# Kernel tuning notes

Measured on AMD Instinct MI355X. Metric: run time of the kernel, lower is better.

Reference implementation:

```python
import jax, jax.numpy as jnp
import numpy as np

N_NODES = 50000
N_EDGES = 800000
IN_DIM = 128
OUT_DIM = 128
NUM_HEADS = 8
HEAD_DIM = OUT_DIM // NUM_HEADS
LN_EPS = 1e-5


def setup_inputs() -> dict:
    key = jax.random.key(0)
    ks = jax.random.split(key, 8)
    # xavier-uniform bounds
    def xavier(k, shape, fan_in, fan_out):
        a = float(np.sqrt(6.0 / (fan_in + fan_out)))
        return jax.random.uniform(k, shape, jnp.float32, -a, a)
    x = jax.random.normal(ks[0], (N_NODES, IN_DIM), jnp.float32)
    edge_index = jax.random.randint(ks[1], (2, N_EDGES), 0, N_NODES, jnp.int32)
    # store Linear weights as (in, out) so forward is x @ W (same math as torch x @ W.T)
    W_src = xavier(ks[2], (IN_DIM, OUT_DIM), IN_DIM, OUT_DIM)
    W_dst = xavier(ks[3], (IN_DIM, OUT_DIM), IN_DIM, OUT_DIM)
    attn = xavier(ks[4], (NUM_HEADS, HEAD_DIM), HEAD_DIM, NUM_HEADS)
    W_out = xavier(ks[5], (OUT_DIM, OUT_DIM), OUT_DIM, OUT_DIM)
    b_out = jnp.zeros((OUT_DIM,), jnp.float32)
    gamma = jnp.ones((OUT_DIM,), jnp.float32)
    beta = jnp.zeros((OUT_DIM,), jnp.float32)
    return {"x": x, "edge_index": edge_index, "W_src": W_src, "W_dst": W_dst,
            "attn": attn, "W_out": W_out, "b_out": b_out, "gamma": gamma, "beta": beta}


def reference(x, edge_index, W_src, W_dst, attn, W_out, b_out, gamma, beta):
    N = x.shape[0]
    H, D = attn.shape
    src, dst = edge_index[0], edge_index[1]
    # node transforms: (N, H, D)
    h_src = (x @ W_src).reshape(N, H, D)
    h_dst = (x @ W_dst).reshape(N, H, D)
    # per-edge GATv2 attention logits (E, H)
    h_src_e = h_src[src]                                  # (E, H, D)
    e = jax.nn.leaky_relu(h_src_e + h_dst[dst], 0.2)
    s = jnp.einsum('ehd,hd->eh', e, attn)
    # segment (scatter) softmax over incoming edges of each dst node
    m = jax.ops.segment_max(s, dst, num_segments=N)       # (N, H)
    exp = jnp.exp(s - m[dst])
    denom = jax.ops.segment_sum(exp, dst, num_segments=N)
    alpha = exp / (denom[dst] + 1e-8)                     # (E, H)
    # weighted message aggregation
    msg = (h_src_e * alpha[..., None]).reshape(-1, H * D)
    out = jax.ops.segment_sum(msg, dst, num_segments=N)   # (N, H*D)
    out = out @ W_out + b_out
    out = out + x                                          # residual (in_dim == out_dim)
    # LayerNorm
    mu = jnp.mean(out, axis=-1, keepdims=True)
    var = jnp.var(out, axis=-1, keepdims=True)
    out = (out - mu) * jax.lax.rsqrt(var + LN_EPS) * gamma + beta
    return out
```

## Files before the change

kernel.cpp:

```cpp
#include <hip/hip_runtime.h>
#include <hip/hip_bf16.h>

#define HEADS 8
#define CDIM 128
#define CAP 96
#define CHUNK 2048
#define CSTR 16
#define LOG2E 1.44269504088896f

typedef __attribute__((ext_vector_type(8))) short bf16x8;
typedef __attribute__((ext_vector_type(4))) float f32x4;
typedef __attribute__((ext_vector_type(2))) _Float16 h16x2;

__device__ __forceinline__ unsigned short f2bs(float f) {
    union { __hip_bfloat16 b; unsigned short u; } c;
    c.b = __float2bfloat16(f);
    return c.u;
}

__device__ __forceinline__ unsigned short f2hs(float f) {
    union { _Float16 h; unsigned short u; } c;
    c.h = (_Float16)f;
    return c.u;
}

__global__ __launch_bounds__(256) void init_kernel(
        int* __restrict__ cnt,
        const float* __restrict__ Wsrc,
        const float* __restrict__ Wdst,
        const float* __restrict__ Wout,
        unsigned short* __restrict__ WT,
        unsigned short* __restrict__ WoT, int N, int nzblk) {
    const int b = blockIdx.x;
    if (b < nzblk) {
        const int i = b * 256 + threadIdx.x;
        if (i < N * CSTR) cnt[i] = 0;
        return;
    }
    const int i = (b - nzblk) * 256 + threadIdx.x;
    if (i < 16384)      { WT[i] = f2bs(Wsrc[(i & 127) * CDIM + (i >> 7)]); }
    else if (i < 32768) { int j = i - 16384; WT[16384 + j] = f2bs(Wdst[(j & 127) * CDIM + (j >> 7)]); }
    else if (i < 49152) { int j = i - 32768; WoT[j] = f2bs(Wout[(j & 127) * CDIM + (j >> 7)]); }
}

__global__ __launch_bounds__(256) void fused_bucket_transform3(
        const int* __restrict__ ei,
        int* __restrict__ cnt,
        int* __restrict__ bucket,
        const float* __restrict__ x,
        const unsigned short* __restrict__ WT,
        unsigned short* __restrict__ hsrc,
        unsigned short* __restrict__ hdst,
        int N, int E, int ngemm, int nbucket) {
    const int g = blockIdx.x;
    const bool is_gemm = ((g % 5) == 4) && ((g / 5) < ngemm);
    if (!is_gemm) {
        const int bid = g - g / 5;
        if (bid >= nbucket) return;
        const int shard = bid & 7;
        const int base = (bid >> 3) * CHUNK + (int)threadIdx.x;
        int d[8], s[8];
#pragma unroll
        for (int q = 0; q < 8; q++) {
            const int idx = base + q * 256;
            const int safe = idx < E ? idx : 0;
            d[q] = ei[E + safe];
            s[q] = ei[safe];
        }
        bool act[8];
        int pos[8];
#pragma unroll
        for (int q = 0; q < 8; q++) {
            const int idx = base + q * 256;
            act[q] = (idx < E) && ((d[q] & 7) == shard);
            pos[q] = CAP;
            if (act[q]) pos[q] = atomicAdd(&cnt[(size_t)d[q] * CSTR], 1);
        }
#pragma unroll
        for (int q = 0; q < 8; q++) {
            if (act[q] && pos[q] < CAP) bucket[(size_t)d[q] * CAP + pos[q]] = s[q];
        }
        return;
    }
    __shared__ unsigned short As[64][136];
    __shared__ unsigned short Bs[128][136];
    const int t = threadIdx.x;
    const int m0 = (g / 5) * 64;
    for (int i = t; i < 64 * 32; i += 256) {
        const int r = i >> 5, kq = i & 31;
        const int gr = m0 + r;
        float4 v = make_float4(0.f, 0.f, 0.f, 0.f);
        if (gr < N) v = *(const float4*)(x + (size_t)gr * CDIM + kq * 4);
        uint2 pk;
        pk.x = (unsigned)f2bs(v.x) | ((unsigned)f2bs(v.y) << 16);
        pk.y = (unsigned)f2bs(v.z) | ((unsigned)f2bs(v.w) << 16);
        *(uint2*)&As[r][kq * 4] = pk;
    }
    const int w = t >> 6, lane = t & 63, l16 = lane & 15, quad = lane >> 4;
    const int wm = (w & 1) * 32, wn = (w >> 1) * 64;
#pragma unroll
    for (int half = 0; half < 2; half++) {
        const unsigned short* Wb = WT + (size_t)half * 16384;
        for (int i = t; i < 128 * 16; i += 256) {
            const int r = i >> 4, q = i & 15;
            *(uint4*)&Bs[r][q * 8] = *(const uint4*)(Wb + (size_t)r * CDIM + q * 8);
        }
        __syncthreads();
        f32x4 acc[2][4];
#pragma unroll
        for (int mi = 0; mi < 2; mi++)
#pragma unroll
            for (int ni = 0; ni < 4; ni++) acc[mi][ni] = (f32x4){0.f, 0.f, 0.f, 0.f};
#pragma unroll
        for (int kc = 0; kc < 4; kc++) {
            const int k0 = kc * 32 + quad * 8;
            bf16x8 af[2], bf[4];
            af[0] = *(const bf16x8*)&As[wm + l16][k0];
            af[1] = *(const bf16x8*)&As[wm + 16 + l16][k0];
#pragma unroll
            for (int ni = 0; ni < 4; ni++)
                bf[ni] = *(const bf16x8*)&Bs[wn + ni * 16 + l16][k0];
#pragma unroll
            for (int mi = 0; mi < 2; mi++)
#pragma unroll
                for (int ni = 0; ni < 4; ni++)
                    acc[mi][ni] = __builtin_amdgcn_mfma_f32_16x16x32_bf16(af[mi], bf[ni], acc[mi][ni], 0, 0, 0);
        }
        unsigned short* H = half ? hdst : hsrc;
#pragma unroll
        for (int mi = 0; mi < 2; mi++)
#pragma unroll
            for (int reg = 0; reg < 4; reg++) {
                const int gm = m0 + wm + mi * 16 + quad * 4 + reg;
                if (gm < N) {
#pragma unroll
                    for (int ni = 0; ni < 4; ni++)
                        H[(size_t)gm * CDIM + wn + ni * 16 + l16] = f2hs(acc[mi][ni][reg]);
                }
            }
        __syncthreads();
    }
}

__global__ __launch_bounds__(256) void attn_agg6(
        const unsigned short* __restrict__ hsrc,
        const unsigned short* __restrict__ hdst,
        const float* __restrict__ attn,
        const int* __restrict__ cnt,
        const int* __restrict__ bucket,
        unsigned short* __restrict__ aggb) {
    __shared__ int src_lds[4][CAP];
    const int t = threadIdx.x;
    const int w = t >> 6, lane = t & 63;
    const int dst = blockIdx.x * 4 + w;
    int deg = cnt[(size_t)dst * CSTR];
    deg = deg > CAP ? CAP : deg;
    for (int j = lane; j < deg; j += 64)
        src_lds[w][j] = bucket[(size_t)dst * CAP + j];

    const int l32 = lane & 31;
    const int eh = lane >> 5;
    const uint2 hdu = *(const uint2*)(hdst + (size_t)dst * CDIM + l32 * 4);
    const h16x2 hd01 = __builtin_bit_cast(h16x2, hdu.x);
    const h16x2 hd23 = __builtin_bit_cast(h16x2, hdu.y);
    const float4 a4 = ((const float4*)attn)[l32];
    h16x2 a01, a23;
    a01[0] = (_Float16)(a4.x * LOG2E); a01[1] = (_Float16)(a4.y * LOG2E);
    a23[0] = (_Float16)(a4.z * LOG2E); a23[1] = (_Float16)(a4.w * LOG2E);
    const h16x2 k02 = { (_Float16)0.2f, (_Float16)0.2f };

    const unsigned short* hb = hsrc + l32 * 4;

    float l = 0.f, acc0 = 0.f, acc1 = 0.f, acc2 = 0.f, acc3 = 0.f;
    for (int j0 = 0; j0 < deg; j0 += 8) {
        uint2 vv[4];
#pragma unroll
        for (int p = 0; p < 4; p++) {
            const int j = j0 + 2 * p + eh;
            const int sj = (j < deg) ? src_lds[w][j] : 0;
            vv[p] = *(const uint2*)(hb + (size_t)sj * CDIM);
        }
#pragma unroll
        for (int p = 0; p < 4; p++) {
            const int j = j0 + 2 * p + eh;
            const h16x2 v01 = __builtin_bit_cast(h16x2, vv[p].x);
            const h16x2 v23 = __builtin_bit_cast(h16x2, vv[p].y);
            h16x2 e01 = v01 + hd01;
            h16x2 e23 = v23 + hd23;
            e01 = __builtin_elementwise_max(e01, e01 * k02);
            e23 = __builtin_elementwise_max(e23, e23 * k02);
            float pp = __builtin_amdgcn_fdot2(e01, a01, 0.f, false);
            pp = __builtin_amdgcn_fdot2(e23, a23, pp, false);
            pp += __int_as_float(__builtin_amdgcn_update_dpp(0, __float_as_int(pp), 0xB1, 0xF, 0xF, true));
            pp += __int_as_float(__builtin_amdgcn_update_dpp(0, __float_as_int(pp), 0x4E, 0xF, 0xF, true));
            float wgt = __builtin_amdgcn_exp2f(pp);
            wgt = (j < deg) ? wgt : 0.f;
            l += wgt;
            acc0 = fmaf(wgt, (float)v01[0], acc0);
            acc1 = fmaf(wgt, (float)v01[1], acc1);
            acc2 = fmaf(wgt, (float)v23[0], acc2);
            acc3 = fmaf(wgt, (float)v23[1], acc3);
        }
    }
    l    += __shfl_xor(l, 32);
    acc0 += __shfl_xor(acc0, 32);
    acc1 += __shfl_xor(acc1, 32);
    acc2 += __shfl_xor(acc2, 32);
    acc3 += __shfl_xor(acc3, 32);
    if (lane < 32) {
        const float r = 1.f / (l + 1e-8f);
        uint2 o;
        o.x = (unsigned)f2bs(acc0 * r) | ((unsigned)f2bs(acc1 * r) << 16);
        o.y = (unsigned)f2bs(acc2 * r) | ((unsigned)f2bs(acc3 * r) << 16);
        *(uint2*)(aggb + (size_t)dst * CDIM + l32 * 4) = o;
    }
}

__global__ __launch_bounds__(256) void out_mfma_ln64(
        const unsigned short* __restrict__ aggb,
        const float* __restrict__ x,
        const unsigned short* __restrict__ WoT,
        const float* __restrict__ bo,
        const float* __restrict__ gam,
        const float* __restrict__ bet,
        float* __restrict__ out, int N) {
    __shared__ unsigned short As[64][136];
    __shared__ unsigned short Bs[128][136];
    __shared__ float red1[64][2], red2[64][2];
    __shared__ float s_mu[64], s_rs[64];
    const int t = threadIdx.x;
    const int m0 = blockIdx.x * 64;
    for (int i = t; i < 64 * 16; i += 256) {
        const int r = i >> 4, q = i & 15;
        const int gr = m0 + r;
        uint4 v = make_uint4(0u, 0u, 0u, 0u);
        if (gr < N) v = *(const uint4*)(aggb + (size_t)gr * CDIM + q * 8);
        *(uint4*)&As[r][q * 8] = v;
    }
    for (int i = t; i < 128 * 16; i += 256) {
        const int r = i >> 4, q = i & 15;
        *(uint4*)&Bs[r][q * 8] = *(const uint4*)(WoT + (size_t)r * CDIM + q * 8);
    }
    __syncthreads();
    const int w = t >> 6, lane = t & 63, l16 = lane & 15, quad = lane >> 4;
    const int wm = (w & 1) * 32, wn = (w >> 1) * 64;
    f32x4 acc[2][4];
#pragma unroll
    for (int mi = 0; mi < 2; mi++)
#pragma unroll
        for (int ni = 0; ni < 4; ni++) acc[mi][ni] = (f32x4){0.f, 0.f, 0.f, 0.f};
#pragma unroll
    for (int kc = 0; kc < 4; kc++) {
        const int k0 = kc * 32 + quad * 8;
        bf16x8 af[2], bf[4];
        af[0] = *(const bf16x8*)&As[l16 + wm][k0];
        af[1] = *(const bf16x8*)&As[l16 + wm + 16][k0];
#pragma unroll
        for (int ni = 0; ni < 4; ni++)
            bf[ni] = *(const bf16x8*)&Bs[wn + ni * 16 + l16][k0];
#pragma unroll
        for (int mi = 0; mi < 2; mi++)
#pragma unroll
            for (int ni = 0; ni < 4; ni++)
                acc[mi][ni] = __builtin_amdgcn_mfma_f32_16x16x32_bf16(af[mi], bf[ni], acc[mi][ni], 0, 0, 0);
    }
    float bi[4], g4[4], be4[4];
#pragma unroll
    for (int ni = 0; ni < 4; ni++) {
        const int n = wn + ni * 16 + l16;
        bi[ni] = bo[n]; g4[ni] = gam[n]; be4[ni] = bet[n];
    }
#pragma unroll
    for (int mi = 0; mi < 2; mi++)
#pragma unroll
        for (int reg = 0; reg < 4; reg++) {
            const int gm = m0 + wm + mi * 16 + quad * 4 + reg;
#pragma unroll
            for (int ni = 0; ni < 4; ni++) {
                const float xr = (gm < N) ? x[(size_t)gm * CDIM + wn + ni * 16 + l16] : 0.f;
                acc[mi][ni][reg] += bi[ni] + xr;
            }
        }
#pragma unroll
    for (int mi = 0; mi < 2; mi++)
#pragma unroll
        for (int reg = 0; reg < 4; reg++) {
            float s1 = acc[mi][0][reg] + acc[mi][1][reg] + acc[mi][2][reg] + acc[mi][3][reg];
            float s2 = acc[mi][0][reg] * acc[mi][0][reg] + acc[mi][1][reg] * acc[mi][1][reg]
                     + acc[mi][2][reg] * acc[mi][2][reg] + acc[mi][3][reg] * acc[mi][3][reg];
            s1 += __shfl_xor(s1, 1, 16); s1 += __shfl_xor(s1, 2, 16);
            s1 += __shfl_xor(s1, 4, 16); s1 += __shfl_xor(s1, 8, 16);
            s2 += __shfl_xor(s2, 1, 16); s2 += __shfl_xor(s2, 2, 16);
            s2 += __shfl_xor(s2, 4, 16); s2 += __shfl_xor(s2, 8, 16);
            if (l16 == 0) {
                const int row = wm + mi * 16 + quad * 4 + reg;
                red1[row][w >> 1] = s1;
                red2[row][w >> 1] = s2;
            }
        }
    __syncthreads();
    if (t < 64) {
        const float s1 = red1[t][0] + red1[t][1];
        const float s2 = red2[t][0] + red2[t][1];
        const float mu = s1 * (1.f / 128.f);
        const float var = s2 * (1.f / 128.f) - mu * mu;
        s_mu[t] = mu;
        s_rs[t] = rsqrtf(var + 1e-5f);
    }
    __syncthreads();
#pragma unroll
    for (int mi = 0; mi < 2; mi++)
#pragma unroll
        for (int reg = 0; reg < 4; reg++) {
            const int row = wm + mi * 16 + quad * 4 + reg;
            const int gm = m0 + row;
            if (gm < N) {
                const float mu = s_mu[row], rs = s_rs[row];
#pragma unroll
                for (int ni = 0; ni < 4; ni++)
                    out[(size_t)gm * CDIM + wn + ni * 16 + l16] =
                        (acc[mi][ni][reg] - mu) * rs * g4[ni] + be4[ni];
            }
        }
}

extern "C" void kernel_launch(void* const* d_in, const int* in_sizes, int n_in,
                              void* d_out, int out_size, void* d_ws, size_t ws_size,
                              hipStream_t stream) {
    const float* x    = (const float*)d_in[0];
    const int*   ei   = (const int*)d_in[1];
    const float* Wsrc = (const float*)d_in[2];
    const float* Wdst = (const float*)d_in[3];
    const float* attn = (const float*)d_in[4];
    const float* Wout = (const float*)d_in[5];
    const float* bo   = (const float*)d_in[6];
    const float* gam  = (const float*)d_in[7];
    const float* bet  = (const float*)d_in[8];
    float* out = (float*)d_out;

    const int N = in_sizes[0] / CDIM;
    const int E = in_sizes[1] / 2;
    const int NX = N * CDIM;

    unsigned short* hsrc_h = (unsigned short*)d_ws;
    unsigned short* hdst_h = hsrc_h + (size_t)NX;
    unsigned short* aggb   = hdst_h + (size_t)NX;
    unsigned short* WT     = aggb + (size_t)NX;
    unsigned short* WoT    = WT + 32768;
    int* cnt    = (int*)(WoT + 16384);
    int* bucket = cnt + (size_t)N * CSTR;

    const int nzblk    = (N * CSTR + 255) / 256;
    const int nwblk    = 49152 / 256;
    const int ngroups  = (E + CHUNK - 1) / CHUNK;
    const int nbucket  = ngroups * 8;
    const int ngemm    = (N + 63) / 64;

    init_kernel<<<nzblk + nwblk, 256, 0, stream>>>(cnt, Wsrc, Wdst, Wout, WT, WoT, N, nzblk);
    fused_bucket_transform3<<<nbucket + ngemm, 256, 0, stream>>>(
        ei, cnt, bucket, x, WT, hsrc_h, hdst_h, N, E, ngemm, nbucket);
    attn_agg6<<<N / 4, 256, 0, stream>>>(hsrc_h, hdst_h, attn, cnt, bucket, aggb);
    out_mfma_ln64<<<(N + 63) / 64, 256, 0, stream>>>(aggb, x, WoT, bo, gam, bet, out, N);
}
```

Baseline: 187.1 us.

## Fuse attention aggregation with output GEMM and LayerNorm kernel

Merges the per-destination attention aggregation kernel into the output projection + LayerNorm kernel, keeping aggregated rows in LDS instead of writing them to global memory. Each wave now loops over 16 destination nodes sequentially, and the output GEMM is restructured so each wave owns 16 rows across all 128 columns, eliminating cross-wave LayerNorm reductions. This removes a kernel launch and the intermediate bf16 round trip, but greatly reduces the number of blocks and serializes the latency-bound gathers within each wave.

```diff
diff --git a/kernel.cpp b/kernel.cpp
--- a/kernel.cpp
+++ b/kernel.cpp
@@ -142,82 +142,12 @@
     }
 }
 
-__global__ __launch_bounds__(256) void attn_agg6(
+__global__ __launch_bounds__(256, 4) void attn_out_fused(
         const unsigned short* __restrict__ hsrc,
         const unsigned short* __restrict__ hdst,
         const float* __restrict__ attn,
         const int* __restrict__ cnt,
         const int* __restrict__ bucket,
-        unsigned short* __restrict__ aggb) {
-    __shared__ int src_lds[4][CAP];
-    const int t = threadIdx.x;
-    const int w = t >> 6, lane = t & 63;
-    const int dst = blockIdx.x * 4 + w;
-    int deg = cnt[(size_t)dst * CSTR];
-    deg = deg > CAP ? CAP : deg;
-    for (int j = lane; j < deg; j += 64)
-        src_lds[w][j] = bucket[(size_t)dst * CAP + j];
-
-    const int l32 = lane & 31;
-    const int eh = lane >> 5;
-    const uint2 hdu = *(const uint2*)(hdst + (size_t)dst * CDIM + l32 * 4);
-    const h16x2 hd01 = __builtin_bit_cast(h16x2, hdu.x);
-    const h16x2 hd23 = __builtin_bit_cast(h16x2, hdu.y);
-    const float4 a4 = ((const float4*)attn)[l32];
-    h16x2 a01, a23;
-    a01[0] = (_Float16)(a4.x * LOG2E); a01[1] = (_Float16)(a4.y * LOG2E);
-    a23[0] = (_Float16)(a4.z * LOG2E); a23[1] = (_Float16)(a4.w * LOG2E);
-    const h16x2 k02 = { (_Float16)0.2f, (_Float16)0.2f };
-
-    const unsigned short* hb = hsrc + l32 * 4;
-
-    float l = 0.f, acc0 = 0.f, acc1 = 0.f, acc2 = 0.f, acc3 = 0.f;
-    for (int j0 = 0; j0 < deg; j0 += 8) {
-        uint2 vv[4];
-#pragma unroll
-        for (int p = 0; p < 4; p++) {
-            const int j = j0 + 2 * p + eh;
-            const int sj = (j < deg) ? src_lds[w][j] : 0;
-            vv[p] = *(const uint2*)(hb + (size_t)sj * CDIM);
-        }
-#pragma unroll
-        for (int p = 0; p < 4; p++) {
-            const int j = j0 + 2 * p + eh;
-            const h16x2 v01 = __builtin_bit_cast(h16x2, vv[p].x);
-            const h16x2 v23 = __builtin_bit_cast(h16x2, vv[p].y);
-            h16x2 e01 = v01 + hd01;
-            h16x2 e23 = v23 + hd23;
-            e01 = __builtin_elementwise_max(e01, e01 * k02);
-            e23 = __builtin_elementwise_max(e23, e23 * k02);
-            float pp = __builtin_amdgcn_fdot2(e01, a01, 0.f, false);
-            pp = __builtin_amdgcn_fdot2(e23, a23, pp, false);
-            pp += __int_as_float(__builtin_amdgcn_update_dpp(0, __float_as_int(pp), 0xB1, 0xF, 0xF, true));
-            pp += __int_as_float(__builtin_amdgcn_update_dpp(0, __float_as_int(pp), 0x4E, 0xF, 0xF, true));
-            float wgt = __builtin_amdgcn_exp2f(pp);
-            wgt = (j < deg) ? wgt : 0.f;
-            l += wgt;
-            acc0 = fmaf(wgt, (float)v01[0], acc0);
-            acc1 = fmaf(wgt, (float)v01[1], acc1);
-            acc2 = fmaf(wgt, (float)v23[0], acc2);
-            acc3 = fmaf(wgt, (float)v23[1], acc3);
-        }
-    }
-    l    += __shfl_xor(l, 32);
-    acc0 += __shfl_xor(acc0, 32);
-    acc1 += __shfl_xor(acc1, 32);
-    acc2 += __shfl_xor(acc2, 32);
-    acc3 += __shfl_xor(acc3, 32);
-    if (lane < 32) {
-        const float r = 1.f / (l + 1e-8f);
-        uint2 o;
-        o.x = (unsigned)f2bs(acc0 * r) | ((unsigned)f2bs(acc1 * r) << 16);
-        o.y = (unsigned)f2bs(acc2 * r) | ((unsigned)f2bs(acc3 * r) << 16);
-        *(uint2*)(aggb + (size_t)dst * CDIM + l32 * 4) = o;
-    }
-}
-
-__global__ __launch_bounds__(256) void out_mfma_ln64(
-        const unsigned short* __restrict__ aggb,
         const float* __restrict__ x,
         const unsigned short* __restrict__ WoT,
         const float* __restrict__ bo,
@@ -225,102 +155,139 @@
         const float* __restrict__ bet,
         float* __restrict__ out, int N) {
     __shared__ unsigned short As[64][136];
-    __shared__ unsigned short Bs[128][136];
-    __shared__ float red1[64][2], red2[64][2];
-    __shared__ float s_mu[64], s_rs[64];
+    __shared__ unsigned short Bs[64][136];
+    __shared__ int src_lds[4][CAP];
     const int t = threadIdx.x;
+    const int w = t >> 6, lane = t & 63, l16 = lane & 15, quad = lane >> 4;
+    const int l32 = lane & 31, eh = lane >> 5;
     const int m0 = blockIdx.x * 64;
-    for (int i = t; i < 64 * 16; i += 256) {
-        const int r = i >> 4, q = i & 15;
-        const int gr = m0 + r;
-        uint4 v = make_uint4(0u, 0u, 0u, 0u);
-        if (gr < N) v = *(const uint4*)(aggb + (size_t)gr * CDIM + q * 8);
-        *(uint4*)&As[r][q * 8] = v;
-    }
-    for (int i = t; i < 128 * 16; i += 256) {
-        const int r = i >> 4, q = i & 15;
-        *(uint4*)&Bs[r][q * 8] = *(const uint4*)(WoT + (size_t)r * CDIM + q * 8);
-    }
-    __syncthreads();
-    const int w = t >> 6, lane = t & 63, l16 = lane & 15, quad = lane >> 4;
-    const int wm = (w & 1) * 32, wn = (w >> 1) * 64;
-    f32x4 acc[2][4];
-#pragma unroll
-    for (int mi = 0; mi < 2; mi++)
-#pragma unroll
-        for (int ni = 0; ni < 4; ni++) acc[mi][ni] = (f32x4){0.f, 0.f, 0.f, 0.f};
-#pragma unroll
-    for (int kc = 0; kc < 4; kc++) {
-        const int k0 = kc * 32 + quad * 8;
-        bf16x8 af[2], bf[4];
-        af[0] = *(const bf16x8*)&As[l16 + wm][k0];
-        af[1] = *(const bf16x8*)&As[l16 + wm + 16][k0];
-#pragma unroll
-        for (int ni = 0; ni < 4; ni++)
-            bf[ni] = *(const bf16x8*)&Bs[wn + ni * 16 + l16][k0];
-#pragma unroll
-        for (int mi = 0; mi < 2; mi++)
+    const int gm0 = m0 + w * 16;
+
+    const float4 a4 = ((const float4*)attn)[l32];
+    h16x2 a01, a23;
+    a01[0] = (_Float16)(a4.x * LOG2E); a01[1] = (_Float16)(a4.y * LOG2E);
+    a23[0] = (_Float16)(a4.z * LOG2E); a23[1] = (_Float16)(a4.w * LOG2E);
+    const h16x2 k02 = { (_Float16)0.2f, (_Float16)0.2f };
+    const unsigned short* hb = hsrc + l32 * 4;
+
+    for (int i = 0; i < 16; i++) {
+        const int dst = gm0 + i;
+        if (dst >= N) break;
+        int deg = cnt[(size_t)dst * CSTR];
+        deg = deg > CAP ? CAP : deg;
+        for (int j = lane; j < deg; j += 64)
+            src_lds[w][j] = bucket[(size_t)dst * CAP + j];
+
+        const uint2 hdu = *(const uint2*)(hdst + (size_t)dst * CDIM + l32 * 4);
+        const h16x2 hd01 = __builtin_bit_cast(h16x2, hdu.x);
+        const h16x2 hd23 = __builtin_bit_cast(h16x2, hdu.y);
+
+        float l = 0.f, acc0 = 0.f, acc1 = 0.f, acc2 = 0.f, acc3 = 0.f;
+        for (int j0 = 0; j0 < deg; j0 += 8) {
+            uint2 vv[4];
+#pragma unroll
+            for (int p = 0; p < 4; p++) {
+                const int j = j0 + 2 * p + eh;
+                const int sj = (j < deg) ? src_lds[w][j] : 0;
+                vv[p] = *(const uint2*)(hb + (size_t)sj * CDIM);
+            }
+#pragma unroll
+            for (int p = 0; p < 4; p++) {
+                const int j = j0 + 2 * p + eh;
+                const h16x2 v01 = __builtin_bit_cast(h16x2, vv[p].x);
+                const h16x2 v23 = __builtin_bit_cast(h16x2, vv[p].y);
+                h16x2 e01 = v01 + hd01;
+                h16x2 e23 = v23 + hd23;
+                e01 = __builtin_elementwise_max(e01, e01 * k02);
+                e23 = __builtin_elementwise_max(e23, e23 * k02);
+                float pp = __builtin_amdgcn_fdot2(e01, a01, 0.f, false);
+                pp = __builtin_amdgcn_fdot2(e23, a23, pp, false);
+                pp += __int_as_float(__builtin_amdgcn_update_dpp(0, __float_as_int(pp), 0xB1, 0xF, 0xF, true));
+                pp += __int_as_float(__builtin_amdgcn_update_dpp(0, __float_as_int(pp), 0x4E, 0xF, 0xF, true));
+                float wgt = __builtin_amdgcn_exp2f(pp);
+                wgt = (j < deg) ? wgt : 0.f;
+                l += wgt;
+                acc0 = fmaf(wgt, (float)v01[0], acc0);
+                acc1 = fmaf(wgt, (float)v01[1], acc1);
+                acc2 = fmaf(wgt, (float)v23[0], acc2);
+                acc3 = fmaf(wgt, (float)v23[1], acc3);
+            }
+        }
+        l    += __shfl_xor(l, 32);
+        acc0 += __shfl_xor(acc0, 32);
+        acc1 += __shfl_xor(acc1, 32);
+        acc2 += __shfl_xor(acc2, 32);
+        acc3 += __shfl_xor(acc3, 32);
+        if (lane < 32) {
+            const float r = 1.f / (l + 1e-8f);
+            uint2 o;
+            o.x = (unsigned)f2bs(acc0 * r) | ((unsigned)f2bs(acc1 * r) << 16);
+            o.y = (unsigned)f2bs(acc2 * r) | ((unsigned)f2bs(acc3 * r) << 16);
+            *(uint2*)&As[w * 16 + i][l32 * 4] = o;
+        }
+    }
+
+    bf16x8 af[4];
+#pragma unroll
+    for (int kc = 0; kc < 4; kc++)
+        af[kc] = *(const bf16x8*)&As[w * 16 + l16][kc * 32 + quad * 8];
+    f32x4 acc[8];
+#pragma unroll
+    for (int a = 0; a < 8; a++) acc[a] = (f32x4){0.f, 0.f, 0.f, 0.f};
+#pragma unroll
+    for (int nb = 0; nb < 2; nb++) {
+        if (nb) __syncthreads();
+        for (int i = t; i < 64 * 16; i += 256) {
+            const int r = i >> 4, q = i & 15;
+            *(uint4*)&Bs[r][q * 8] = *(const uint4*)(WoT + (size_t)(nb * 64 + r) * CDIM + q * 8);
+        }
+        __syncthreads();
+#pragma unroll
+        for (int kc = 0; kc < 4; kc++) {
+            const int k0 = kc * 32 + quad * 8;
+            bf16x8 bf[4];
 #pragma unroll
             for (int ni = 0; ni < 4; ni++)
-                acc[mi][ni] = __builtin_amdgcn_mfma_f32_16x16x32_bf16(af[mi], bf[ni], acc[mi][ni], 0, 0, 0);
-    }
-    float bi[4], g4[4], be4[4];
-#pragma unroll
-    for (int ni = 0; ni < 4; ni++) {
-        const int n = wn + ni * 16 + l16;
-        bi[ni] = bo[n]; g4[ni] = gam[n]; be4[ni] = bet[n];
-    }
-#pragma unroll
-    for (int mi = 0; mi < 2; mi++)
+                bf[ni] = *(const bf16x8*)&Bs[ni * 16 + l16][k0];
+#pragma unroll
+            for (int ni = 0; ni < 4; ni++)
+                acc[nb * 4 + ni] = __builtin_amdgcn_mfma_f32_16x16x32_bf16(af[kc], bf[ni], acc[nb * 4 + ni], 0, 0, 0);
+        }
+    }
+    float g4[8], be4[8];
+#pragma unroll
+    for (int a = 0; a < 8; a++) {
+        const int n = a * 16 + l16;
+        const float bi = bo[n]; g4[a] = gam[n]; be4[a] = bet[n];
 #pragma unroll
         for (int reg = 0; reg < 4; reg++) {
-            const int gm = m0 + wm + mi * 16 + quad * 4 + reg;
-#pragma unroll
-            for (int ni = 0; ni < 4; ni++) {
-                const float xr = (gm < N) ? x[(size_t)gm * CDIM + wn + ni * 16 + l16] : 0.f;
-                acc[mi][ni][reg] += bi[ni] + xr;
-            }
-        }
-#pragma unroll
-    for (int mi = 0; mi < 2; mi++)
+            const int gm = gm0 + quad * 4 + reg;
+            const float xr = (gm < N) ? x[(size_t)gm * CDIM + n] : 0.f;
+            acc[a][reg] += bi + xr;
+        }
+    }
+    float mu4[4], rs4[4];
+#pragma unroll
+    for (int reg = 0; reg < 4; reg++) {
+        float s1 = 0.f, s2 = 0.f;
+#pragma unroll
+        for (int a = 0; a < 8; a++) { s1 += acc[a][reg]; s2 += acc[a][reg] * acc[a][reg]; }
+        s1 += __shfl_xor(s1, 1, 16); s1 += __shfl_xor(s1, 2, 16);
+        s1 += __shfl_xor(s1, 4, 16); s1 += __shfl_xor(s1, 8, 16);
+        s2 += __shfl_xor(s2, 1, 16); s2 += __shfl_xor(s2, 2, 16);
+        s2 += __shfl_xor(s2, 4, 16); s2 += __shfl_xor(s2, 8, 16);
+        const float mu = s1 * (1.f / 128.f);
+        mu4[reg] = mu;
+        rs4[reg] = rsqrtf(s2 * (1.f / 128.f) - mu * mu + 1e-5f);
+    }
+#pragma unroll
+    for (int a = 0; a < 8; a++)
 #pragma unroll
         for (int reg = 0; reg < 4; reg++) {
-            float s1 = acc[mi][0][reg] + acc[mi][1][reg] + acc[mi][2][reg] + acc[mi][3][reg];
-            float s2 = acc[mi][0][reg] * acc[mi][0][reg] + acc[mi][1][reg] * acc[mi][1][reg]
-                     + acc[mi][2][reg] * acc[mi][2][reg] + acc[mi][3][reg] * acc[mi][3][reg];
-            s1 += __shfl_xor(s1, 1, 16); s1 += __shfl_xor(s1, 2, 16);
-            s1 += __shfl_xor(s1, 4, 16); s1 += __shfl_xor(s1, 8, 16);
-            s2 += __shfl_xor(s2, 1, 16); s2 += __shfl_xor(s2, 2, 16);
-            s2 += __shfl_xor(s2, 4, 16); s2 += __shfl_xor(s2, 8, 16);
-            if (l16 == 0) {
-                const int row = wm + mi * 16 + quad * 4 + reg;
-                red1[row][w >> 1] = s1;
-                red2[row][w >> 1] = s2;
-            }
-        }
-    __syncthreads();
-    if (t < 64) {
-        const float s1 = red1[t][0] + red1[t][1];
-        const float s2 = red2[t][0] + red2[t][1];
-        const float mu = s1 * (1.f / 128.f);
-        const float var = s2 * (1.f / 128.f) - mu * mu;
-        s_mu[t] = mu;
-        s_rs[t] = rsqrtf(var + 1e-5f);
-    }
-    __syncthreads();
-#pragma unroll
-    for (int mi = 0; mi < 2; mi++)
-#pragma unroll
-        for (int reg = 0; reg < 4; reg++) {
-            const int row = wm + mi * 16 + quad * 4 + reg;
-            const int gm = m0 + row;
-            if (gm < N) {
-                const float mu = s_mu[row], rs = s_rs[row];
-#pragma unroll
-                for (int ni = 0; ni < 4; ni++)
-                    out[(size_t)gm * CDIM + wn + ni * 16 + l16] =
-                        (acc[mi][ni][reg] - mu) * rs * g4[ni] + be4[ni];
-            }
+            const int gm = gm0 + quad * 4 + reg;
+            if (gm < N)
+                out[(size_t)gm * CDIM + a * 16 + l16] =
+                    (acc[a][reg] - mu4[reg]) * rs4[reg] * g4[a] + be4[a];
         }
 }
 
@@ -349,6 +316,7 @@
     unsigned short* WoT    = WT + 32768;
     int* cnt    = (int*)(WoT + 16384);
     int* bucket = cnt + (size_t)N * CSTR;
+    (void)aggb;
 
     const int nzblk    = (N * CSTR + 255) / 256;
     const int nwblk    = 49152 / 256;
@@ -359,6 +327,6 @@
     init_kernel<<<nzblk + nwblk, 256, 0, stream>>>(cnt, Wsrc, Wdst, Wout, WT, WoT, N, nzblk);
     fused_bucket_transform3<<<nbucket + ngemm, 256, 0, stream>>>(
         ei, cnt, bucket, x, WT, hsrc_h, hdst_h, N, E, ngemm, nbucket);
-    attn_agg6<<<N / 4, 256, 0, stream>>>(hsrc_h, hdst_h, attn, cnt, bucket, aggb);
-    out_mfma_ln64<<<(N + 63) / 64, 256, 0, stream>>>(aggb, x, WoT, bo, gam, bet, out, N);
-}
+    attn_out_fused<<<(N + 63) / 64, 256, 0, stream>>>(
+        hsrc_h, hdst_h, attn, cnt, bucket, x, WoT, bo, gam, bet, out, N);
+}
```

New measurement: 191.2 us. +2.2%, slower.
